# Performance work log

Hardware: AMD Instinct MI355X
Metric: run time of the kernel (lower is better)

Reference implementation:

```python
import jax, jax.numpy as jnp
import numpy as np

# 4D conv over (L, P, W, H) decomposed as k shifted 3D convs over (P, W, H),
# with the L spatial dim folded into the batch. Faithful to convNd(num_dims=4),
# stride 1, 'same' padding (padding = (k-1)//2), no bias.

def conv4d(x, w):
    # x: [B, C, L, P, W, H]; w: [O, I, k, k, k, k]
    k = w.shape[2]
    p = (k - 1) // 2
    B, C, L, P, Wd, Hd = x.shape
    O = w.shape[0]
    xp = jnp.pad(x, ((0, 0), (0, 0), (p, p), (0, 0), (0, 0), (0, 0)))
    dn = ('NCDHW', 'OIDHW', 'NCDHW')
    out = jnp.zeros((B, O, L, P, Wd, Hd), x.dtype)
    for dl in range(k):  # k <= 3, static loop over kernel taps along L
        xs = xp[:, :, dl:dl + L]                                  # [B,C,L,P,W,H]
        xs = xs.transpose(0, 2, 1, 3, 4, 5).reshape(B * L, C, P, Wd, Hd)
        y = jax.lax.conv_general_dilated(xs, w[:, :, dl], (1, 1, 1),
                                         [(p, p)] * 3, dimension_numbers=dn)
        out = out + y.reshape(B, L, O, P, Wd, Hd).transpose(0, 2, 1, 3, 4, 5)
    return out


def inception4d(x, weights):
    # mean over parallel 4D convs with kernel sizes 1, 3, ... (2i+1)
    acc = conv4d(x, weights[0])
    for w in weights[1:]:
        acc = acc + conv4d(x, w)
    return acc / len(weights)


def setup_inputs() -> dict:
    key = jax.random.key(0)
    ks = jax.random.split(key, 5)
    B, T, W, H, C = 4, 48, 8, 8, 32
    d_model, d_ff = 32, 64
    x = jax.random.normal(ks[0], (B, T, W, H, C), dtype=jnp.float32)
    # Inception_Block4D weights: kernel sizes 1 and 3 (num_kernels=2), no bias
    w1_0 = jax.random.normal(ks[1], (d_ff, d_model, 1, 1, 1, 1), dtype=jnp.float32) * 0.1
    w1_1 = jax.random.normal(ks[2], (d_ff, d_model, 3, 3, 3, 3), dtype=jnp.float32) * 0.02
    w2_0 = jax.random.normal(ks[3], (d_model, d_ff, 1, 1, 1, 1), dtype=jnp.float32) * 0.1
    w2_1 = jax.random.normal(ks[4], (d_model, d_ff, 3, 3, 3, 3), dtype=jnp.float32) * 0.02
    return {"x": x, "w1_0": w1_0, "w1_1": w1_1, "w2_0": w2_0, "w2_1": w2_1}


def reference(x, w1_0, w1_1, w2_0, w2_1):
    B, T, W, H, C = x.shape
    periods = (2, 3, 4)                       # FFT_for_Period hardcoded output
    xf = jnp.ones((B, len(periods)), x.dtype) # hardcoded uniform weights
    real_len = T                              # seq_len + pred_len
    res = []
    for period in periods:
        if real_len % period != 0:
            length = (real_len // period + 1) * period
            out = jnp.concatenate([x, x[:, -(length - real_len):]], axis=1)
        else:
            length = real_len
            out = x
        # [B, L, P, W, H, C] -> [B, C, L, P, W, H]
        out = out.reshape(B, length // period, period, W, H, C).transpose(0, 5, 1, 2, 3, 4)
        h = inception4d(out, [w1_0, w1_1])
        h = jax.nn.gelu(h, approximate=False)  # torch nn.GELU default (exact)
        h = inception4d(h, [w2_0, w2_1])
        # [B, C, L, P, W, H] -> [B, (L P), W, H, C]
        h = h.transpose(0, 2, 3, 4, 5, 1).reshape(B, length, W, H, C)
        res.append(h[:, :real_len])
    res = jnp.stack(res, axis=1)              # [B, k, T, W, H, C]
    pw = jax.nn.softmax(xf, axis=1).reshape(B, len(periods), 1, 1, 1, 1)
    return jnp.sum(res * pw, axis=1) + x
```

## Files before the change

kernel.cpp:

```cpp
#include <hip/hip_runtime.h>
#include <math.h>


typedef __attribute__((ext_vector_type(8))) short bf16x8;
typedef __attribute__((ext_vector_type(4))) float f32x4;
typedef unsigned short u16;

#define XC 3200
#define HC2 7168
#define XSEG 617600
#define ZSEG_END 639104
#define W1OFF 639104
#define W2OFF 804992
#define H1OFF 970880
#define H1P 1383424
#define PREP_N 970880
#define OUT_Q 98304
#define PREP_TOT (PREP_N + OUT_Q)

#define WAITVM(N) asm volatile("s_waitcnt vmcnt(" #N ")" ::: "memory")
#define SBAR()    asm volatile("s_barrier" ::: "memory")

__device__ __forceinline__ u16 f2bf(float f) {
    unsigned u = __float_as_uint(f);
    unsigned r = u + 0x7fffu + ((u >> 16) & 1u);
    return (u16)(r >> 16);
}
__device__ __forceinline__ float gelu_exact(float v) {
    return 0.5f * v * (1.0f + erff(v * 0.7071067811865476f));
}

__device__ __forceinline__ void cp1k(const u16* g, u16* l, int lane) {
    __builtin_amdgcn_global_load_lds(
        (const __attribute__((address_space(1))) unsigned int*)(g + lane * 8),
        (__attribute__((address_space(3))) unsigned int*)(l + lane * 8),
        16, 0, 0);
}

__global__ __launch_bounds__(256) void prep(
    const float* __restrict__ x,
    const float* __restrict__ w1_0, const float* __restrict__ w1_1,
    const float* __restrict__ w2_0, const float* __restrict__ w2_1,
    u16* __restrict__ ws, float* __restrict__ out) {
    int i = blockIdx.x * 256 + threadIdx.x;
    if (i < XSEG) {
        int cellidx = i / XC; int inner = i - cellidx * XC;
        int cellpos = inner >> 5; int low = inner & 31;
        int sc = low >> 3, jj = low & 7;
        int c = ((sc ^ (cellpos & 3)) << 3) + jj;
        int wp = cellpos / 10, hp = cellpos - (cellpos / 10) * 10;
        float v = 0.f;
        if (cellidx < 192 && wp >= 1 && wp <= 8 && hp >= 1 && hp <= 8)
            v = x[(cellidx * 64 + (wp - 1) * 8 + (hp - 1)) * 32 + c];
        ws[i] = f2bf(v);
    } else if (i < ZSEG_END) {
        int j = i - XSEG;
        int per = j / 7168; int off = j - per * 7168;
        ws[H1OFF + per * H1P + 192 * 7168 + off] = 0;
    } else if (i < W2OFF) {
        int j = i - W1OFF;
        int tap = j >> 11; int r = j & 2047;
        int nh = r >> 10; int rr = r & 1023;
        int chunkh = rr >> 3, jj = rr & 7;
        int m = chunkh & 15, nq = (chunkh >> 4) & 1, quad = chunkh >> 5;
        int o = nh * 32 + nq * 16 + m, c = quad * 8 + jj;
        float v = 0.5f * w1_1[(o * 32 + c) * 81 + tap];
        if (tap == 40) v += 0.5f * w1_0[o * 32 + c];
        ws[i] = f2bf(v);
    } else if (i < PREP_N) {
        int j = i - W2OFF;
        int tap = j >> 11; int r = j & 2047;
        int kh = r >> 10; int rr = r & 1023;
        int chunkh = rr >> 3, jj = rr & 7;
        int m = chunkh & 15, nt = (chunkh >> 4) & 1, quad = chunkh >> 5;
        int o = nt * 16 + m, c = kh * 32 + quad * 8 + jj;
        float v = 0.5f * w2_1[(o * 64 + c) * 81 + tap];
        if (tap == 40) v += 0.5f * w2_0[o * 64 + c];
        ws[i] = f2bf(v);
    } else if (i < PREP_TOT) {
        int j = i - PREP_N;
        ((float4*)out)[j] = ((const float4*)x)[j];
    }
}

template<int P>
__device__ __forceinline__ int cidx(int bb, int l2, int q2) {
    constexpr int L = 48 / P;
    return ((unsigned)l2 < (unsigned)L && (unsigned)q2 < (unsigned)P)
               ? bb * 48 + l2 * P + q2 : 192;
}

template<int P>
__device__ __forceinline__ void conv1_body(
    const u16* __restrict__ xs, const u16* __restrict__ w1b,
    u16* __restrict__ h1, int tp, int bb, int nh,
    u16* __restrict__ s_a, u16* __restrict__ s_w) {
    constexpr int HB = (P == 2) ? 0 : (P == 3) ? H1P : 2 * H1P;

    int tid = threadIdx.x;
    int lane = tid & 63, wv = tid >> 6;
    int m = lane & 15, quad = lane >> 4;
    int t0 = tp * 2, t = t0 + wv;
    int l = t / P, q = t - l * P;

    int sp[4];
#pragma unroll
    for (int mtl = 0; mtl < 4; ++mtl) {
        int pos = mtl * 16 + m;
        sp[mtl] = (pos >> 3) * 10 + (pos & 7);
    }

    f32x4 acc[4][2];
#pragma unroll
    for (int mtl = 0; mtl < 4; ++mtl)
#pragma unroll
        for (int nq = 0; nq < 2; ++nq) acc[mtl][nq] = f32x4{0.f, 0.f, 0.f, 0.f};

    const u16* ba = s_a + wv * 3584;

#pragma unroll 1
    for (int g = 0; g < 9; ++g) {
        int dl = g / 3, dq = g - dl * 3;
        const u16* ac = xs + cidx<P>(bb, l + dl - 1, q + dq - 1) * XC;
        u16* ad = s_a + wv * 3584;
#pragma unroll
        for (int i = 0; i < 7; ++i)
            cp1k(ac + i * 512, ad + i * 512, lane);
#pragma unroll
        for (int i = 0; i < 9; ++i) {
            int k = wv * 9 + i;
            cp1k(w1b + (g * 9 + (k >> 1)) * 2048 + nh * 1024 + (k & 1) * 512,
                 s_w + k * 512, lane);
        }
        WAITVM(0); SBAR();

#pragma unroll
        for (int pj = 0; pj < 9; ++pj) {
            int dw = pj / 3, dh = pj - (pj / 3) * 3;
            const u16* tw = s_w + pj * 1024;
            bf16x8 wf0 = *(const bf16x8*)(tw + (((quad * 2 + 0) * 16 + m) << 3));
            bf16x8 wf1 = *(const bf16x8*)(tw + (((quad * 2 + 1) * 16 + m) << 3));
#pragma unroll
            for (int mtl = 0; mtl < 4; ++mtl) {
                int cellpos = sp[mtl] + dw * 10 + dh;
                bf16x8 af = *(const bf16x8*)(ba + cellpos * 32 +
                                             ((quad ^ (cellpos & 3)) << 3));
                acc[mtl][0] = __builtin_amdgcn_mfma_f32_16x16x32_bf16(
                    af, wf0, acc[mtl][0], 0, 0, 0);
                acc[mtl][1] = __builtin_amdgcn_mfma_f32_16x16x32_bf16(
                    af, wf1, acc[mtl][1], 0, 0, 0);
            }
        }
        if (g < 8) SBAR();
    }

    u16* hh = h1 + HB + (bb * 48 + t) * HC2 + nh * 3584;
#pragma unroll
    for (int mtl = 0; mtl < 4; ++mtl)
#pragma unroll
        for (int r = 0; r < 4; ++r) {
            int pos = mtl * 16 + quad * 4 + r;
            int cellpos = ((pos >> 3) + 1) * 10 + (pos & 7) + 1;
#pragma unroll
            for (int nq = 0; nq < 2; ++nq) {
                int ol = nq * 16 + m;
                hh[cellpos * 32 + (((ol >> 3) ^ (cellpos & 3)) << 3) + (ol & 7)] =
                    f2bf(gelu_exact(acc[mtl][nq][r]));
            }
        }
#pragma unroll
    for (int it = 0; it < 9; ++it) {
        int k = it * 128 + tid;
        int tb = k >= 576; int rr = k - tb * 576;
        int bp = rr >> 4, u = rr & 15;
        int cp;
        if (bp < 10) cp = bp;
        else if (bp < 20) cp = 90 + (bp - 10);
        else if (bp < 28) cp = (bp - 19) * 10;
        else cp = (bp - 27) * 10 + 9;
        unsigned int* h32 = (unsigned int*)(h1 + HB +
            (bb * 48 + t0 + tb) * HC2 + nh * 3584);
        h32[cp * 16 + u] = 0;
    }
}

__global__ __launch_bounds__(128, 2) void conv1_k(
    const u16* __restrict__ ws_x, const u16* __restrict__ ws_w1,
    u16* __restrict__ ws_h1) {
    __shared__ __align__(16) u16 s_a[2 * 3584];
    __shared__ __align__(16) u16 s_w[18 * 512];
    int g = blockIdx.x;
    int jid = (g & 7) * 72 + (g >> 3);
    int per = jid / 192; int rem = jid - per * 192;
    int bb = rem / 48; int r2 = rem - bb * 48;
    int tp = r2 >> 1, nh = r2 & 1;
    if (per == 0)      conv1_body<2>(ws_x, ws_w1, ws_h1, tp, bb, nh, s_a, s_w);
    else if (per == 1) conv1_body<3>(ws_x, ws_w1, ws_h1, tp, bb, nh, s_a, s_w);
    else               conv1_body<4>(ws_x, ws_w1, ws_h1, tp, bb, nh, s_a, s_w);
}

template<int P>
__device__ __forceinline__ void conv2_body(
    const u16* __restrict__ h1, const u16* __restrict__ w2b,
    float* __restrict__ out, int tp, int bb, int kh,
    u16* __restrict__ s_a, u16* __restrict__ s_w) {
    constexpr int HB = (P == 2) ? 0 : (P == 3) ? H1P : 2 * H1P;

    int tid = threadIdx.x;
    int lane = tid & 63, wv = tid >> 6;
    int m = lane & 15, quad = lane >> 4;
    int t0 = tp * 2, t = t0 + wv;
    int l = t / P, q = t - l * P;
    const u16* hb = h1 + HB;

    int sp[4];
#pragma unroll
    for (int mtl = 0; mtl < 4; ++mtl) {
        int pos = mtl * 16 + m;
        sp[mtl] = (pos >> 3) * 10 + (pos & 7);
    }

    f32x4 acc[4][2];
#pragma unroll
    for (int mtl = 0; mtl < 4; ++mtl)
#pragma unroll
        for (int nt = 0; nt < 2; ++nt) acc[mtl][nt] = f32x4{0.f, 0.f, 0.f, 0.f};

    const u16* ba = s_a + wv * 3584;

#pragma unroll 1
    for (int g = 0; g < 9; ++g) {
        int dl = g / 3, dq = g - dl * 3;
        const u16* ac = hb + cidx<P>(bb, l + dl - 1, q + dq - 1) * HC2 +
                        kh * 3584;
        u16* ad = s_a + wv * 3584;
#pragma unroll
        for (int i = 0; i < 7; ++i)
            cp1k(ac + i * 512, ad + i * 512, lane);
#pragma unroll
        for (int i = 0; i < 9; ++i) {
            int k = wv * 9 + i;
            cp1k(w2b + (g * 9 + (k >> 1)) * 2048 + kh * 1024 + (k & 1) * 512,
                 s_w + k * 512, lane);
        }
        WAITVM(0); SBAR();

#pragma unroll
        for (int pj = 0; pj < 9; ++pj) {
            int dw = pj / 3, dh = pj - (pj / 3) * 3;
            const u16* tw = s_w + pj * 1024;
            bf16x8 wf0 = *(const bf16x8*)(tw + (((quad * 2 + 0) * 16 + m) << 3));
            bf16x8 wf1 = *(const bf16x8*)(tw + (((quad * 2 + 1) * 16 + m) << 3));
#pragma unroll
            for (int mtl = 0; mtl < 4; ++mtl) {
                int cellpos = sp[mtl] + dw * 10 + dh;
                bf16x8 af = *(const bf16x8*)(ba + cellpos * 32 +
                                             ((quad ^ (cellpos & 3)) << 3));
                acc[mtl][0] = __builtin_amdgcn_mfma_f32_16x16x32_bf16(
                    af, wf0, acc[mtl][0], 0, 0, 0);
                acc[mtl][1] = __builtin_amdgcn_mfma_f32_16x16x32_bf16(
                    af, wf1, acc[mtl][1], 0, 0, 0);
            }
        }
        if (g < 8) SBAR();
    }

    float* orow = out + (bb * 48 + t) * 2048;
    const float s = 1.0f / 3.0f;
#pragma unroll
    for (int mtl = 0; mtl < 4; ++mtl)
#pragma unroll
        for (int nt = 0; nt < 2; ++nt)
#pragma unroll
            for (int r = 0; r < 4; ++r) {
                int pos = mtl * 16 + quad * 4 + r;
                atomicAdd(&orow[pos * 32 + nt * 16 + m], acc[mtl][nt][r] * s);
            }
}

__global__ __launch_bounds__(128, 2) void conv2_k(
    const u16* __restrict__ ws_h1, const u16* __restrict__ ws_w2,
    float* __restrict__ out) {
    __shared__ __align__(16) u16 s_a[2 * 3584];
    __shared__ __align__(16) u16 s_w[18 * 512];
    int g = blockIdx.x;
    int jid = (g & 7) * 72 + (g >> 3);
    int per = jid / 192; int rem = jid - per * 192;
    int bb = rem / 48; int r2 = rem - bb * 48;
    int tp = r2 >> 1, kh = r2 & 1;
    if (per == 0)      conv2_body<2>(ws_h1, ws_w2, out, tp, bb, kh, s_a, s_w);
    else if (per == 1) conv2_body<3>(ws_h1, ws_w2, out, tp, bb, kh, s_a, s_w);
    else               conv2_body<4>(ws_h1, ws_w2, out, tp, bb, kh, s_a, s_w);
}

extern "C" void kernel_launch(void* const* d_in, const int* in_sizes, int n_in,
                              void* d_out, int out_size, void* d_ws, size_t ws_size,
                              hipStream_t stream) {
    const float* x    = (const float*)d_in[0];
    const float* w1_0 = (const float*)d_in[1];
    const float* w1_1 = (const float*)d_in[2];
    const float* w2_0 = (const float*)d_in[3];
    const float* w2_1 = (const float*)d_in[4];
    float* out = (float*)d_out;

    u16* ws = (u16*)d_ws;
    u16* ws_x  = ws;
    u16* ws_w1 = ws + W1OFF;
    u16* ws_w2 = ws + W2OFF;
    u16* ws_h1 = ws + H1OFF;

    prep<<<(PREP_TOT + 255) / 256, 256, 0, stream>>>(
        x, w1_0, w1_1, w2_0, w2_1, ws, out);
    conv1_k<<<576, 128, 0, stream>>>(ws_x, ws_w1, ws_h1);
    conv2_k<<<576, 128, 0, stream>>>(ws_h1, ws_w2, out);
}
```

Baseline: 121.3 us.

## Stage shared halo of time slices once per block and pipeline weight loads

Each block now covers 6 consecutive time steps with 12 waves, two waves per step each handling half the spatial rows. All neighbouring (L,P) slices plus a zero slice are loaded into LDS once up front, so the 9 taps no longer each reload their activation slice. Weights are streamed in 27 chunks through a 4-deep ring buffer, so the copy of the next chunk overlaps the MFMA work on the current one. The grid drops from 576 to 192 blocks with much more LDS per block, which lowers the number of resident blocks and the parallelism on the machine.

Measured after the change: 118.9 us. 2.0% less time.

```diff
diff --git a/kernel.cpp b/kernel.cpp
--- a/kernel.cpp
+++ b/kernel.cpp
@@ -84,65 +84,82 @@
 }
 
 template<int P>
-__device__ __forceinline__ int cidx(int bb, int l2, int q2) {
-    constexpr int L = 48 / P;
-    return ((unsigned)l2 < (unsigned)L && (unsigned)q2 < (unsigned)P)
-               ? bb * 48 + l2 * P + q2 : 192;
-}
-
-template<int P>
 __device__ __forceinline__ void conv1_body(
     const u16* __restrict__ xs, const u16* __restrict__ w1b,
-    u16* __restrict__ h1, int tp, int bb, int nh,
+    u16* __restrict__ h1, int tpp, int bb, int nh,
     u16* __restrict__ s_a, u16* __restrict__ s_w) {
     constexpr int HB = (P == 2) ? 0 : (P == 3) ? H1P : 2 * H1P;
+    constexpr int L = 48 / P;
+    constexpr int EXT = P + 1;
+    constexpr int NW = 6 + 2 * EXT;
+    constexpr int ZS = NW;
+    constexpr int NP = (NW + 1) * 7;
 
     int tid = threadIdx.x;
     int lane = tid & 63, wv = tid >> 6;
     int m = lane & 15, quad = lane >> 4;
-    int t0 = tp * 2, t = t0 + wv;
+    int ts = wv >> 1, mh = wv & 1;
+    int t0 = tpp * 6, t = t0 + ts;
     int l = t / P, q = t - l * P;
 
-    int sp[4];
-#pragma unroll
-    for (int mtl = 0; mtl < 4; ++mtl) {
-        int pos = mtl * 16 + m;
+    int sp[2];
+#pragma unroll
+    for (int mtl = 0; mtl < 2; ++mtl) {
+        int pos = (mh * 2 + mtl) * 16 + m;
         sp[mtl] = (pos >> 3) * 10 + (pos & 7);
     }
 
-    f32x4 acc[4][2];
-#pragma unroll
-    for (int mtl = 0; mtl < 4; ++mtl)
+    f32x4 acc[2][2];
+#pragma unroll
+    for (int mtl = 0; mtl < 2; ++mtl)
 #pragma unroll
         for (int nq = 0; nq < 2; ++nq) acc[mtl][nq] = f32x4{0.f, 0.f, 0.f, 0.f};
 
-    const u16* ba = s_a + wv * 3584;
+    for (int p = wv; p < NP; p += 12) {
+        int si = p / 7, pc = p - si * 7;
+        int tt = t0 - EXT + si;
+        int cell = (si == ZS) ? 192
+                 : (((unsigned)tt < 48u) ? bb * 48 + tt : 192);
+        cp1k(xs + cell * XC + pc * 512, s_a + si * 3584 + pc * 512, lane);
+    }
+    if (wv < 6) {
+        cp1k(w1b + (0 * 3 + (wv >> 1)) * 2048 + nh * 1024 + (wv & 1) * 512,
+             s_w + 0 * 3072 + wv * 512, lane);
+        cp1k(w1b + (1 * 3 + (wv >> 1)) * 2048 + nh * 1024 + (wv & 1) * 512,
+             s_w + 1 * 3072 + wv * 512, lane);
+        WAITVM(1);
+    } else {
+        WAITVM(0);
+    }
+    SBAR();
 
 #pragma unroll 1
-    for (int g = 0; g < 9; ++g) {
-        int dl = g / 3, dq = g - dl * 3;
-        const u16* ac = xs + cidx<P>(bb, l + dl - 1, q + dq - 1) * XC;
-        u16* ad = s_a + wv * 3584;
-#pragma unroll
-        for (int i = 0; i < 7; ++i)
-            cp1k(ac + i * 512, ad + i * 512, lane);
-#pragma unroll
-        for (int i = 0; i < 9; ++i) {
-            int k = wv * 9 + i;
-            cp1k(w1b + (g * 9 + (k >> 1)) * 2048 + nh * 1024 + (k & 1) * 512,
-                 s_w + k * 512, lane);
-        }
-        WAITVM(0); SBAR();
-
-#pragma unroll
-        for (int pj = 0; pj < 9; ++pj) {
-            int dw = pj / 3, dh = pj - (pj / 3) * 3;
-            const u16* tw = s_w + pj * 1024;
+    for (int cg = 0; cg < 27; ++cg) {
+        if (wv < 6 && cg < 25)
+            cp1k(w1b + ((cg + 2) * 3 + (wv >> 1)) * 2048 + nh * 1024 +
+                     (wv & 1) * 512,
+                 s_w + ((cg + 2) & 3) * 3072 + wv * 512, lane);
+        if (cg < 25)       { WAITVM(2); }
+        else if (cg == 25) { WAITVM(1); }
+        else               { WAITVM(0); }
+        SBAR();
+
+        int g2 = cg / 3, dw = cg - g2 * 3;
+        int dl = g2 / 3, dq = g2 - dl * 3;
+        int lq = l + dl - 1, qq = q + dq - 1;
+        bool valid = ((unsigned)lq < (unsigned)L) &&
+                     ((unsigned)qq < (unsigned)P);
+        int si = valid ? (ts + dl * P + dq) : ZS;
+        const u16* ba = s_a + si * 3584;
+        const u16* bw = s_w + (cg & 3) * 3072;
+#pragma unroll
+        for (int j = 0; j < 3; ++j) {
+            const u16* tw = bw + j * 1024;
             bf16x8 wf0 = *(const bf16x8*)(tw + (((quad * 2 + 0) * 16 + m) << 3));
             bf16x8 wf1 = *(const bf16x8*)(tw + (((quad * 2 + 1) * 16 + m) << 3));
 #pragma unroll
-            for (int mtl = 0; mtl < 4; ++mtl) {
-                int cellpos = sp[mtl] + dw * 10 + dh;
+            for (int mtl = 0; mtl < 2; ++mtl) {
+                int cellpos = sp[mtl] + dw * 10 + j;
                 bf16x8 af = *(const bf16x8*)(ba + cellpos * 32 +
                                              ((quad ^ (cellpos & 3)) << 3));
                 acc[mtl][0] = __builtin_amdgcn_mfma_f32_16x16x32_bf16(
@@ -151,15 +168,14 @@
                     af, wf1, acc[mtl][1], 0, 0, 0);
             }
         }
-        if (g < 8) SBAR();
     }
 
     u16* hh = h1 + HB + (bb * 48 + t) * HC2 + nh * 3584;
 #pragma unroll
-    for (int mtl = 0; mtl < 4; ++mtl)
+    for (int mtl = 0; mtl < 2; ++mtl)
 #pragma unroll
         for (int r = 0; r < 4; ++r) {
-            int pos = mtl * 16 + quad * 4 + r;
+            int pos = (mh * 2 + mtl) * 16 + quad * 4 + r;
             int cellpos = ((pos >> 3) + 1) * 10 + (pos & 7) + 1;
 #pragma unroll
             for (int nq = 0; nq < 2; ++nq) {
@@ -169,91 +185,117 @@
             }
         }
 #pragma unroll
-    for (int it = 0; it < 9; ++it) {
-        int k = it * 128 + tid;
-        int tb = k >= 576; int rr = k - tb * 576;
-        int bp = rr >> 4, u = rr & 15;
-        int cp;
-        if (bp < 10) cp = bp;
-        else if (bp < 20) cp = 90 + (bp - 10);
-        else if (bp < 28) cp = (bp - 19) * 10;
-        else cp = (bp - 27) * 10 + 9;
-        unsigned int* h32 = (unsigned int*)(h1 + HB +
-            (bb * 48 + t0 + tb) * HC2 + nh * 3584);
-        h32[cp * 16 + u] = 0;
-    }
-}
-
-__global__ __launch_bounds__(128, 2) void conv1_k(
+    for (int it = 0; it < 5; ++it) {
+        int k = it * 768 + tid;
+        if (k < 3456) {
+            int tc = k / 576; int rr = k - tc * 576;
+            int bp = rr >> 4, u = rr & 15;
+            int cp;
+            if (bp < 10) cp = bp;
+            else if (bp < 20) cp = 90 + (bp - 10);
+            else if (bp < 28) cp = (bp - 19) * 10;
+            else cp = (bp - 27) * 10 + 9;
+            unsigned int* h32 = (unsigned int*)(h1 + HB +
+                (bb * 48 + t0 + tc) * HC2 + nh * 3584);
+            h32[cp * 16 + u] = 0;
+        }
+    }
+}
+
+__global__ __launch_bounds__(768) void conv1_k(
     const u16* __restrict__ ws_x, const u16* __restrict__ ws_w1,
     u16* __restrict__ ws_h1) {
-    __shared__ __align__(16) u16 s_a[2 * 3584];
-    __shared__ __align__(16) u16 s_w[18 * 512];
+    __shared__ __align__(16) u16 s_a[17 * 3584];
+    __shared__ __align__(16) u16 s_w[4 * 3072];
     int g = blockIdx.x;
-    int jid = (g & 7) * 72 + (g >> 3);
-    int per = jid / 192; int rem = jid - per * 192;
-    int bb = rem / 48; int r2 = rem - bb * 48;
-    int tp = r2 >> 1, nh = r2 & 1;
-    if (per == 0)      conv1_body<2>(ws_x, ws_w1, ws_h1, tp, bb, nh, s_a, s_w);
-    else if (per == 1) conv1_body<3>(ws_x, ws_w1, ws_h1, tp, bb, nh, s_a, s_w);
-    else               conv1_body<4>(ws_x, ws_w1, ws_h1, tp, bb, nh, s_a, s_w);
+    int jid = (g & 7) * 24 + (g >> 3);
+    int per = jid / 64; int rem = jid - per * 64;
+    int bb = rem / 16; int r2 = rem - bb * 16;
+    int tpp = r2 >> 1, nh = r2 & 1;
+    if (per == 0)      conv1_body<2>(ws_x, ws_w1, ws_h1, tpp, bb, nh, s_a, s_w);
+    else if (per == 1) conv1_body<3>(ws_x, ws_w1, ws_h1, tpp, bb, nh, s_a, s_w);
+    else               conv1_body<4>(ws_x, ws_w1, ws_h1, tpp, bb, nh, s_a, s_w);
 }
 
 template<int P>
 __device__ __forceinline__ void conv2_body(
     const u16* __restrict__ h1, const u16* __restrict__ w2b,
-    float* __restrict__ out, int tp, int bb, int kh,
+    float* __restrict__ out, int tpp, int bb, int kh,
     u16* __restrict__ s_a, u16* __restrict__ s_w) {
     constexpr int HB = (P == 2) ? 0 : (P == 3) ? H1P : 2 * H1P;
+    constexpr int L = 48 / P;
+    constexpr int EXT = P + 1;
+    constexpr int NW = 6 + 2 * EXT;
+    constexpr int ZS = NW;
+    constexpr int NP = (NW + 1) * 7;
 
     int tid = threadIdx.x;
     int lane = tid & 63, wv = tid >> 6;
     int m = lane & 15, quad = lane >> 4;
-    int t0 = tp * 2, t = t0 + wv;
+    int ts = wv >> 1, mh = wv & 1;
+    int t0 = tpp * 6, t = t0 + ts;
     int l = t / P, q = t - l * P;
     const u16* hb = h1 + HB;
 
-    int sp[4];
-#pragma unroll
-    for (int mtl = 0; mtl < 4; ++mtl) {
-        int pos = mtl * 16 + m;
+    int sp[2];
+#pragma unroll
+    for (int mtl = 0; mtl < 2; ++mtl) {
+        int pos = (mh * 2 + mtl) * 16 + m;
         sp[mtl] = (pos >> 3) * 10 + (pos & 7);
     }
 
-    f32x4 acc[4][2];
-#pragma unroll
-    for (int mtl = 0; mtl < 4; ++mtl)
+    f32x4 acc[2][2];
+#pragma unroll
+    for (int mtl = 0; mtl < 2; ++mtl)
 #pragma unroll
         for (int nt = 0; nt < 2; ++nt) acc[mtl][nt] = f32x4{0.f, 0.f, 0.f, 0.f};
 
-    const u16* ba = s_a + wv * 3584;
+    for (int p = wv; p < NP; p += 12) {
+        int si = p / 7, pc = p - si * 7;
+        int tt = t0 - EXT + si;
+        int cell = (si == ZS) ? 192
+                 : (((unsigned)tt < 48u) ? bb * 48 + tt : 192);
+        cp1k(hb + cell * HC2 + kh * 3584 + pc * 512,
+             s_a + si * 3584 + pc * 512, lane);
+    }
+    if (wv < 6) {
+        cp1k(w2b + (0 * 3 + (wv >> 1)) * 2048 + kh * 1024 + (wv & 1) * 512,
+             s_w + 0 * 3072 + wv * 512, lane);
+        cp1k(w2b + (1 * 3 + (wv >> 1)) * 2048 + kh * 1024 + (wv & 1) * 512,
+             s_w + 1 * 3072 + wv * 512, lane);
+        WAITVM(1);
+    } else {
+        WAITVM(0);
+    }
+    SBAR();
 
 #pragma unroll 1
-    for (int g = 0; g < 9; ++g) {
-        int dl = g / 3, dq = g - dl * 3;
-        const u16* ac = hb + cidx<P>(bb, l + dl - 1, q + dq - 1) * HC2 +
-                        kh * 3584;
-        u16* ad = s_a + wv * 3584;
-#pragma unroll
-        for (int i = 0; i < 7; ++i)
-            cp1k(ac + i * 512, ad + i * 512, lane);
-#pragma unroll
-        for (int i = 0; i < 9; ++i) {
-            int k = wv * 9 + i;
-            cp1k(w2b + (g * 9 + (k >> 1)) * 2048 + kh * 1024 + (k & 1) * 512,
-                 s_w + k * 512, lane);
-        }
-        WAITVM(0); SBAR();
-
-#pragma unroll
-        for (int pj = 0; pj < 9; ++pj) {
-            int dw = pj / 3, dh = pj - (pj / 3) * 3;
-            const u16* tw = s_w + pj * 1024;
+    for (int cg = 0; cg < 27; ++cg) {
+        if (wv < 6 && cg < 25)
+            cp1k(w2b + ((cg + 2) * 3 + (wv >> 1)) * 2048 + kh * 1024 +
+                     (wv & 1) * 512,
+                 s_w + ((cg + 2) & 3) * 3072 + wv * 512, lane);
+        if (cg < 25)       { WAITVM(2); }
+        else if (cg == 25) { WAITVM(1); }
+        else               { WAITVM(0); }
+        SBAR();
+
+        int g2 = cg / 3, dw = cg - g2 * 3;
+        int dl = g2 / 3, dq = g2 - dl * 3;
+        int lq = l + dl - 1, qq = q + dq - 1;
+        bool valid = ((unsigned)lq < (unsigned)L) &&
+                     ((unsigned)qq < (unsigned)P);
+        int si = valid ? (ts + dl * P + dq) : ZS;
+        const u16* ba = s_a + si * 3584;
+        const u16* bw = s_w + (cg & 3) * 3072;
+#pragma unroll
+        for (int j = 0; j < 3; ++j) {
+            const u16* tw = bw + j * 1024;
             bf16x8 wf0 = *(const bf16x8*)(tw + (((quad * 2 + 0) * 16 + m) << 3));
             bf16x8 wf1 = *(const bf16x8*)(tw + (((quad * 2 + 1) * 16 + m) << 3));
 #pragma unroll
-            for (int mtl = 0; mtl < 4; ++mtl) {
-                int cellpos = sp[mtl] + dw * 10 + dh;
+            for (int mtl = 0; mtl < 2; ++mtl) {
+                int cellpos = sp[mtl] + dw * 10 + j;
                 bf16x8 af = *(const bf16x8*)(ba + cellpos * 32 +
                                              ((quad ^ (cellpos & 3)) << 3));
                 acc[mtl][0] = __builtin_amdgcn_mfma_f32_16x16x32_bf16(
@@ -262,35 +304,34 @@
                     af, wf1, acc[mtl][1], 0, 0, 0);
             }
         }
-        if (g < 8) SBAR();
     }
 
     float* orow = out + (bb * 48 + t) * 2048;
     const float s = 1.0f / 3.0f;
 #pragma unroll
-    for (int mtl = 0; mtl < 4; ++mtl)
+    for (int mtl = 0; mtl < 2; ++mtl)
 #pragma unroll
         for (int nt = 0; nt < 2; ++nt)
 #pragma unroll
             for (int r = 0; r < 4; ++r) {
-                int pos = mtl * 16 + quad * 4 + r;
+                int pos = (mh * 2 + mtl) * 16 + quad * 4 + r;
                 atomicAdd(&orow[pos * 32 + nt * 16 + m], acc[mtl][nt][r] * s);
             }
 }
 
-__global__ __launch_bounds__(128, 2) void conv2_k(
+__global__ __launch_bounds__(768) void conv2_k(
     const u16* __restrict__ ws_h1, const u16* __restrict__ ws_w2,
     float* __restrict__ out) {
-    __shared__ __align__(16) u16 s_a[2 * 3584];
-    __shared__ __align__(16) u16 s_w[18 * 512];
+    __shared__ __align__(16) u16 s_a[17 * 3584];
+    __shared__ __align__(16) u16 s_w[4 * 3072];
     int g = blockIdx.x;
-    int jid = (g & 7) * 72 + (g >> 3);
-    int per = jid / 192; int rem = jid - per * 192;
-    int bb = rem / 48; int r2 = rem - bb * 48;
-    int tp = r2 >> 1, kh = r2 & 1;
-    if (per == 0)      conv2_body<2>(ws_h1, ws_w2, out, tp, bb, kh, s_a, s_w);
-    else if (per == 1) conv2_body<3>(ws_h1, ws_w2, out, tp, bb, kh, s_a, s_w);
-    else               conv2_body<4>(ws_h1, ws_w2, out, tp, bb, kh, s_a, s_w);
+    int jid = (g & 7) * 24 + (g >> 3);
+    int per = jid / 64; int rem = jid - per * 64;
+    int bb = rem / 16; int r2 = rem - bb * 16;
+    int tpp = r2 >> 1, kh = r2 & 1;
+    if (per == 0)      conv2_body<2>(ws_h1, ws_w2, out, tpp, bb, kh, s_a, s_w);
+    else if (per == 1) conv2_body<3>(ws_h1, ws_w2, out, tpp, bb, kh, s_a, s_w);
+    else               conv2_body<4>(ws_h1, ws_w2, out, tpp, bb, kh, s_a, s_w);
 }
 
 extern "C" void kernel_launch(void* const* d_in, const int* in_sizes, int n_in,
@@ -311,6 +352,6 @@
 
     prep<<<(PREP_TOT + 255) / 256, 256, 0, stream>>>(
         x, w1_0, w1_1, w2_0, w2_1, ws, out);
-    conv1_k<<<576, 128, 0, stream>>>(ws_x, ws_w1, ws_h1);
-    conv2_k<<<576, 128, 0, stream>>>(ws_h1, ws_w2, out);
-}
+    conv1_k<<<192, 768, 0, stream>>>(ws_x, ws_w1, ws_h1);
+    conv2_k<<<192, 768, 0, stream>>>(ws_h1, ws_w2, out);
+}
```
